# Performance work log

Measured on AMD Instinct MI355X. Metric: run time of the kernel, lower is better.

## Reference

```python
import jax, jax.numpy as jnp
import numpy as np
from jax.ops import segment_sum, segment_max

N = 50000   # nodes
E = 800000  # directed edges
H, C = 4, 64  # GAT heads, per-head channels (hidden_dim//4)
HID = 256
EPS = 1e-5


def setup_inputs() -> dict:
    key = jax.random.key(0)
    ks = jax.random.split(key, 24)
    g = lambda k, shape, fan: jax.random.normal(k, shape, jnp.float32) * (1.0 / np.sqrt(fan))
    inp = {
        'x': jax.random.normal(ks[0], (N, 3), jnp.float32),
        'edge_index': jax.random.randint(ks[1], (2, E), 0, N, jnp.int32),
        # GCNConv 1: 3 -> 64
        'W1': g(ks[2], (3, 64), 3), 'b1': jnp.zeros((64,), jnp.float32),
        # GCNConv 2: 64 -> 128
        'W2': g(ks[3], (64, 128), 64), 'b2': jnp.zeros((128,), jnp.float32),
        # GATConv: 128 -> 4 heads x 64
        'Wg': g(ks[4], (128, H * C), 128),
        'a_src': g(ks[5], (H, C), C), 'a_dst': g(ks[6], (H, C), C),
        'bg': jnp.zeros((H * C,), jnp.float32),
        # LayerNorms
        'ln1_g': jnp.ones((64,), jnp.float32), 'ln1_b': jnp.zeros((64,), jnp.float32),
        'ln2_g': jnp.ones((128,), jnp.float32), 'ln2_b': jnp.zeros((128,), jnp.float32),
        'ln3_g': jnp.ones((HID,), jnp.float32), 'ln3_b': jnp.zeros((HID,), jnp.float32),
        # GlobalAttention gate: Linear(256,256) ReLU Linear(256,1)
        'Wgt1': g(ks[7], (HID, HID), HID), 'bgt1': jnp.zeros((HID,), jnp.float32),
        'Wgt2': g(ks[8], (HID, 1), HID), 'bgt2': jnp.zeros((1,), jnp.float32),
        # output mlp: Linear(256,256) ReLU
        'Wm': g(ks[9], (HID, HID), HID), 'bm': jnp.zeros((HID,), jnp.float32),
    }
    return inp


def _ln(x, g, b):
    mu = x.mean(-1, keepdims=True)
    var = ((x - mu) ** 2).mean(-1, keepdims=True)
    return g * (x - mu) * jax.lax.rsqrt(var + EPS) + b


def reference(x, edge_index, W1, b1, W2, b2, Wg, a_src, a_dst, bg,
              ln1_g, ln1_b, ln2_g, ln2_b, ln3_g, ln3_b,
              Wgt1, bgt1, Wgt2, bgt2, Wm, bm):
    n = x.shape[0]
    loop = jnp.arange(n, dtype=edge_index.dtype)
    src = jnp.concatenate([edge_index[0], loop])  # self-loops added (PyG default)
    dst = jnp.concatenate([edge_index[1], loop])

    # symmetric GCN normalization (deg counts self-loop)
    deg = segment_sum(jnp.ones_like(src, jnp.float32), dst, num_segments=n)
    dinv = jax.lax.rsqrt(jnp.maximum(deg, 1.0))
    norm = (dinv[src] * dinv[dst])[:, None]  # [E+N,1]

    def gcn(h, W, b):
        h = h @ W
        return segment_sum(norm * h[src], dst, num_segments=n) + b

    x1 = _ln(jax.nn.relu(gcn(x, W1, b1)), ln1_g, ln1_b)
    x2 = _ln(jax.nn.relu(gcn(x1, W2, b2)), ln2_g, ln2_b)

    # GATConv: per-head scores, segment-softmax over destination
    h = (x2 @ Wg).reshape(n, H, C)
    s_src = (h * a_src).sum(-1)  # [N,H]
    s_dst = (h * a_dst).sum(-1)
    e = jax.nn.leaky_relu(s_src[src] + s_dst[dst], 0.2)  # [E+N,H]
    m = segment_max(e, dst, num_segments=n)
    ex = jnp.exp(e - m[dst])
    den = segment_sum(ex, dst, num_segments=n)
    alpha = ex / (den[dst] + 1e-16)  # [E+N,H]
    agg = segment_sum(alpha[:, :, None] * h[src], dst, num_segments=n)  # [N,H,C]
    x3 = _ln(agg.reshape(n, H * C) + bg, ln3_g, ln3_b)

    # GlobalAttention pooling (batch=None -> single graph)
    gate = jax.nn.relu(x3 @ Wgt1 + bgt1) @ Wgt2 + bgt2  # [N,1]
    w = jax.nn.softmax(gate, axis=0)
    pooled = (w * x3).sum(0, keepdims=True)  # [1,256]
    out = jax.nn.relu(pooled @ Wm + bm)  # [1,256]
    return out, x3
```

## Files before the change

### kernel.cpp

```cpp
#include <hip/hip_runtime.h>
#include <math.h>

#define NNODES 50000
#define NEDGES 800000

__device__ __forceinline__ float wave_sum(float v) {
#pragma unroll
  for (int o = 32; o > 0; o >>= 1) v += __shfl_xor(v, o, 64);
  return v;
}
__device__ __forceinline__ float wave_max(float v) {
#pragma unroll
  for (int o = 32; o > 0; o >>= 1) v = fmaxf(v, __shfl_xor(v, o, 64));
  return v;
}
template <int NW>
__device__ __forceinline__ float block_sum(float v, float* red) {
  v = wave_sum(v);
  __syncthreads();
  if ((threadIdx.x & 63) == 0) red[threadIdx.x >> 6] = v;
  __syncthreads();
  float s = 0.f;
#pragma unroll
  for (int i = 0; i < NW; i++) s += red[i];
  return s;
}

__device__ __forceinline__ float leaky02(float x) { return x > 0.f ? x : 0.2f * x; }

__device__ __forceinline__ void atomicMaxFloat(float* addr, float val) {
  if (val >= 0.f)
    atomicMax((int*)addr, __float_as_int(val));
  else
    atomicMin((unsigned int*)addr, __float_as_uint(val));
}

__global__ void k_init(int* __restrict__ deg, float* __restrict__ scal,
                       float* __restrict__ pooled) {
  int i = blockIdx.x * blockDim.x + threadIdx.x;
  if (i < NNODES) deg[i] = 0;
  if (i < 256) pooled[i] = 0.f;
  if (i == 0) { scal[0] = -3.0e38f; scal[1] = 0.f; }
}

__global__ void k_deg(const int* __restrict__ dst, int* __restrict__ deg) {
  int e = blockIdx.x * blockDim.x + threadIdx.x;
  if (e < NEDGES) atomicAdd(&deg[dst[e]], 1);
}

__global__ __launch_bounds__(1024) void k_scan(const int* __restrict__ deg,
                                               int* __restrict__ offs,
                                               int* __restrict__ cursor,
                                               float* __restrict__ dinv) {
  __shared__ int lds[1024];
  const int t = threadIdx.x;
  const int chunk = (NNODES + 1023) / 1024;
  int lo = t * chunk, hi = min(lo + chunk, NNODES);
  int s = 0;
  for (int i = lo; i < hi; i++) s += deg[i];
  lds[t] = s;
  __syncthreads();
  for (int off = 1; off < 1024; off <<= 1) {
    int v = (t >= off) ? lds[t - off] : 0;
    __syncthreads();
    lds[t] += v;
    __syncthreads();
  }
  int base = (t > 0) ? lds[t - 1] : 0;
  for (int i = lo; i < hi; i++) {
    int d = deg[i];
    offs[i] = base;
    cursor[i] = base;
    dinv[i] = rsqrtf((float)(d + 1));
    base += d;
  }
  if (t == 1023) offs[NNODES] = lds[1023];
}

__global__ void k_fill(const int* __restrict__ src, const int* __restrict__ dst,
                       int* __restrict__ cursor, int* __restrict__ csr) {
  int e = blockIdx.x * blockDim.x + threadIdx.x;
  if (e >= NEDGES) return;
  int d = dst[e];
  int p = atomicAdd(&cursor[d], 1);
  csr[p] = src[e];
}

__global__ void k_agg3(const float* __restrict__ x, const float* __restrict__ dinv,
                       const int* __restrict__ offs, const int* __restrict__ csr,
                       float* __restrict__ agg0) {
  int n = blockIdx.x * blockDim.x + threadIdx.x;
  if (n >= NNODES) return;
  float di = dinv[n];
  float a0 = di * x[n * 3], a1 = di * x[n * 3 + 1], a2 = di * x[n * 3 + 2];
  int lo = offs[n], hi = offs[n + 1];
  int p = lo;
  int snext = (p < hi) ? csr[p] : 0;
  while (p < hi) {
    int s = snext; p++; if (p < hi) snext = csr[p];
    float w = dinv[s];
    a0 = fmaf(w, x[s * 3], a0);
    a1 = fmaf(w, x[s * 3 + 1], a1);
    a2 = fmaf(w, x[s * 3 + 2], a2);
  }
  agg0[n * 3] = di * a0; agg0[n * 3 + 1] = di * a1; agg0[n * 3 + 2] = di * a2;
}

template <int VEC, int NG>
__global__ __launch_bounds__(64 * NG) void k_agg(const float* __restrict__ h,
                                                 const float* __restrict__ dinv,
                                                 const int* __restrict__ offs,
                                                 const int* __restrict__ csr,
                                                 float* __restrict__ out) {
  __shared__ float lacc[NG][64][VEC + 1];
  const int n = blockIdx.x;
  const int lane = threadIdx.x & 63, g = threadIdx.x >> 6;
  const float di = dinv[n];
  float acc[VEC];
#pragma unroll
  for (int v = 0; v < VEC; v++) acc[v] = 0.f;
  if (g == 0) {
    const float* r = h + (size_t)n * (64 * VEC) + lane * VEC;
#pragma unroll
    for (int v = 0; v < VEC; v++) acc[v] = di * r[v];
  }
  const int lo = offs[n], hi = offs[n + 1];
  int p = lo + g;
  int snext = (p < hi) ? csr[p] : 0;
  while (p < hi) {
    int s = snext; p += NG; if (p < hi) snext = csr[p];
    float w = dinv[s];
    const float* r = h + (size_t)s * (64 * VEC) + lane * VEC;
#pragma unroll
    for (int v = 0; v < VEC; v++) acc[v] = fmaf(w, r[v], acc[v]);
  }
#pragma unroll
  for (int v = 0; v < VEC; v++) lacc[g][lane][v] = acc[v];
  __syncthreads();
  if (g == 0) {
#pragma unroll
    for (int G = 1; G < NG; G++)
#pragma unroll
      for (int v = 0; v < VEC; v++) acc[v] += lacc[G][lane][v];
    float* o = out + (size_t)n * (64 * VEC) + lane * VEC;
#pragma unroll
    for (int v = 0; v < VEC; v++) o[v] = di * acc[v];
  }
}

template <int K, int M, int NT, bool RELU>
__global__ void k_mlp(const float* __restrict__ X, const float* __restrict__ W,
                      const float* __restrict__ b, const float* __restrict__ gam,
                      const float* __restrict__ bet, float* __restrict__ Y) {
  constexpr int NW = M / 64;
  __shared__ float xs[NT * K];
  __shared__ float red[NW];
  const int n0 = blockIdx.x * NT;
  const int j = threadIdx.x;
  const float4* Xt = (const float4*)(X + (size_t)n0 * K);
  for (int i = j; i < NT * K / 4; i += M) ((float4*)xs)[i] = Xt[i];
  __syncthreads();
  float acc[NT];
  float bj = b[j];
#pragma unroll
  for (int r = 0; r < NT; r++) acc[r] = bj;
  for (int k = 0; k < K; k++) {
    float wk = W[k * M + j];
#pragma unroll
    for (int r = 0; r < NT; r++) acc[r] = fmaf(xs[r * K + k], wk, acc[r]);
  }
  float gj = gam[j], btj = bet[j];
  for (int r = 0; r < NT; r++) {
    float a = RELU ? fmaxf(acc[r], 0.f) : acc[r];
    float mu = block_sum<NW>(a, red) * (1.f / M);
    float d = a - mu;
    float var = block_sum<NW>(d * d, red) * (1.f / M);
    Y[(size_t)(n0 + r) * M + j] = fmaf(gj * d, rsqrtf(var + 1e-5f), btj);
  }
}

__global__ void k_uvec(const float* __restrict__ Wg, const float* __restrict__ a_src,
                       const float* __restrict__ a_dst, float* __restrict__ u) {
  const int t = threadIdx.x;
  const int hh = t >> 7, k = t & 127;
  float us = 0.f, ud = 0.f;
  for (int c = 0; c < 64; c++) {
    float w = Wg[k * 256 + hh * 64 + c];
    us = fmaf(w, a_src[hh * 64 + c], us);
    ud = fmaf(w, a_dst[hh * 64 + c], ud);
  }
  u[t] = us;
  u[512 + t] = ud;
}

__global__ __launch_bounds__(256) void k_scores(const float* __restrict__ x2,
                                                const float* __restrict__ u,
                                                float* __restrict__ ssrc,
                                                float* __restrict__ sdst) {
  __shared__ float us[1024];
  const int t = threadIdx.x;
  for (int i = t; i < 1024; i += 256) us[i] = u[i];
  __syncthreads();
  const int n = blockIdx.x * 4 + (t >> 6);
  const int lane = t & 63;
  if (n >= NNODES) return;
  float2 xv = *(const float2*)(x2 + (size_t)n * 128 + lane * 2);
  float d[8];
#pragma unroll
  for (int h = 0; h < 4; h++) {
    d[h] = xv.x * us[h * 128 + lane * 2] + xv.y * us[h * 128 + lane * 2 + 1];
    d[4 + h] = xv.x * us[512 + h * 128 + lane * 2] + xv.y * us[512 + h * 128 + lane * 2 + 1];
  }
#pragma unroll
  for (int o = 32; o > 0; o >>= 1) {
#pragma unroll
    for (int i = 0; i < 8; i++) d[i] += __shfl_xor(d[i], o, 64);
  }
  if (lane == 0) {
    *(float4*)(ssrc + (size_t)n * 4) = make_float4(d[0], d[1], d[2], d[3]);
    *(float4*)(sdst + (size_t)n * 4) = make_float4(d[4], d[5], d[6], d[7]);
  }
}

__global__ __launch_bounds__(256) void k_gatagg(const float* __restrict__ x2,
                                                const float* __restrict__ ssrc,
                                                const float* __restrict__ sdst,
                                                const int* __restrict__ offs,
                                                const int* __restrict__ csr,
                                                float* __restrict__ aggx, int nbase) {
  __shared__ float lm[4][4];
  __shared__ float lden[4][4];
  __shared__ float lacc[4][64][9];
  const int n = nbase + blockIdx.x;
  const int t = threadIdx.x;
  const int lane = t & 63, g = t >> 6;
  const float4 sd = *(const float4*)(sdst + (size_t)n * 4);
  const int lo = offs[n], hi = offs[n + 1];
  float m0 = -3.4e38f, m1 = -3.4e38f, m2 = -3.4e38f, m3 = -3.4e38f;
  float e0x = 0.f, e0y = 0.f, e0z = 0.f, e0w = 0.f;
  if (g == 0) {
    float4 s0 = *(const float4*)(ssrc + (size_t)n * 4);
    e0x = leaky02(s0.x + sd.x); e0y = leaky02(s0.y + sd.y);
    e0z = leaky02(s0.z + sd.z); e0w = leaky02(s0.w + sd.w);
    m0 = e0x; m1 = e0y; m2 = e0z; m3 = e0w;
  }
  for (int p = lo + g; p < hi; p += 4) {
    int s = csr[p];
    float4 ss = *(const float4*)(ssrc + (size_t)s * 4);
    m0 = fmaxf(m0, leaky02(ss.x + sd.x));
    m1 = fmaxf(m1, leaky02(ss.y + sd.y));
    m2 = fmaxf(m2, leaky02(ss.z + sd.z));
    m3 = fmaxf(m3, leaky02(ss.w + sd.w));
  }
  if (lane == 0) { lm[g][0] = m0; lm[g][1] = m1; lm[g][2] = m2; lm[g][3] = m3; }
  __syncthreads();
  const float M0 = fmaxf(fmaxf(lm[0][0], lm[1][0]), fmaxf(lm[2][0], lm[3][0]));
  const float M1 = fmaxf(fmaxf(lm[0][1], lm[1][1]), fmaxf(lm[2][1], lm[3][1]));
  const float M2 = fmaxf(fmaxf(lm[0][2], lm[1][2]), fmaxf(lm[2][2], lm[3][2]));
  const float M3 = fmaxf(fmaxf(lm[0][3], lm[1][3]), fmaxf(lm[2][3], lm[3][3]));
  float den0 = 0.f, den1 = 0.f, den2 = 0.f, den3 = 0.f;
  float a0x = 0.f, a0y = 0.f, a1x = 0.f, a1y = 0.f;
  float a2x = 0.f, a2y = 0.f, a3x = 0.f, a3y = 0.f;
  if (g == 0) {
    float2 xv = *(const float2*)(x2 + (size_t)n * 128 + lane * 2);
    float w;
    w = __expf(e0x - M0); den0 = w; a0x = w * xv.x; a0y = w * xv.y;
    w = __expf(e0y - M1); den1 = w; a1x = w * xv.x; a1y = w * xv.y;
    w = __expf(e0z - M2); den2 = w; a2x = w * xv.x; a2y = w * xv.y;
    w = __expf(e0w - M3); den3 = w; a3x = w * xv.x; a3y = w * xv.y;
  }
  int p = lo + g;
  int snext = (p < hi) ? csr[p] : 0;
  while (p < hi) {
    int s = snext; p += 4; if (p < hi) snext = csr[p];
    float4 ss = *(const float4*)(ssrc + (size_t)s * 4);
    float2 xv = *(const float2*)(x2 + (size_t)s * 128 + lane * 2);
    float w0 = __expf(leaky02(ss.x + sd.x) - M0);
    float w1 = __expf(leaky02(ss.y + sd.y) - M1);
    float w2 = __expf(leaky02(ss.z + sd.z) - M2);
    float w3 = __expf(leaky02(ss.w + sd.w) - M3);
    den0 += w0; den1 += w1; den2 += w2; den3 += w3;
    a0x = fmaf(w0, xv.x, a0x); a0y = fmaf(w0, xv.y, a0y);
    a1x = fmaf(w1, xv.x, a1x); a1y = fmaf(w1, xv.y, a1y);
    a2x = fmaf(w2, xv.x, a2x); a2y = fmaf(w2, xv.y, a2y);
    a3x = fmaf(w3, xv.x, a3x); a3y = fmaf(w3, xv.y, a3y);
  }
  if (lane == 0) { lden[g][0] = den0; lden[g][1] = den1; lden[g][2] = den2; lden[g][3] = den3; }
  lacc[g][lane][0] = a0x; lacc[g][lane][1] = a0y;
  lacc[g][lane][2] = a1x; lacc[g][lane][3] = a1y;
  lacc[g][lane][4] = a2x; lacc[g][lane][5] = a2y;
  lacc[g][lane][6] = a3x; lacc[g][lane][7] = a3y;
  __syncthreads();
  float den = lden[0][g] + lden[1][g] + lden[2][g] + lden[3][g] + 1e-16f;
  float ax = lacc[0][lane][2 * g] + lacc[1][lane][2 * g] + lacc[2][lane][2 * g] + lacc[3][lane][2 * g];
  float ay = lacc[0][lane][2 * g + 1] + lacc[1][lane][2 * g + 1] + lacc[2][lane][2 * g + 1] + lacc[3][lane][2 * g + 1];
  float2 ov; ov.x = ax / den; ov.y = ay / den;
  *(float2*)(aggx + (size_t)blockIdx.x * 512 + g * 128 + lane * 2) = ov;
}

__global__ __launch_bounds__(256) void k_proj(const float* __restrict__ aggx,
                                              const float* __restrict__ Wg,
                                              const float* __restrict__ bg,
                                              const float* __restrict__ gam,
                                              const float* __restrict__ bet,
                                              float* __restrict__ x3, int nbase,
                                              int nrows) {
  __shared__ float xs[16][4 * 132];
  const int r0 = blockIdx.x * 16;
  const int t = threadIdx.x;
  const int cq = t & 63, rq = t >> 6;
  const int h = cq >> 4;
  for (int idx = t; idx < 16 * 128; idx += 256) {
    int r = idx >> 7;
    int p = (idx & 127) << 2;
    int hh = p >> 7, k = p & 127;
    float4 v = (r0 + r < nrows)
                   ? *(const float4*)(aggx + (size_t)(r0 + r) * 512 + p)
                   : make_float4(0.f, 0.f, 0.f, 0.f);
    *(float4*)&xs[r][hh * 132 + k] = v;
  }
  __syncthreads();
  float acc[4][4];
#pragma unroll
  for (int i = 0; i < 4; i++)
#pragma unroll
    for (int j = 0; j < 4; j++) acc[i][j] = 0.f;
  const float4* Wv = (const float4*)Wg;
  for (int k0 = 0; k0 < 128; k0 += 4) {
    float4 xk[4], wk[4];
#pragma unroll
    for (int i = 0; i < 4; i++)
      xk[i] = *(const float4*)&xs[rq * 4 + i][h * 132 + k0];
#pragma unroll
    for (int kk = 0; kk < 4; kk++) wk[kk] = Wv[(size_t)(k0 + kk) * 64 + cq];
#pragma unroll
    for (int kk = 0; kk < 4; kk++) {
      const float* wf = (const float*)&wk[kk];
#pragma unroll
      for (int i = 0; i < 4; i++) {
        const float* xf = (const float*)&xk[i];
        float xv = xf[kk];
#pragma unroll
        for (int j = 0; j < 4; j++) acc[i][j] = fmaf(xv, wf[j], acc[i][j]);
      }
    }
  }
  float4 bgv = *(const float4*)(bg + cq * 4);
  float4 gav = *(const float4*)(gam + cq * 4);
  float4 bev = *(const float4*)(bet + cq * 4);
  const float* bgf = (const float*)&bgv;
  const float* gaf = (const float*)&gav;
  const float* bef = (const float*)&bev;
#pragma unroll
  for (int i = 0; i < 4; i++) {
    float a[4], s = 0.f;
#pragma unroll
    for (int j = 0; j < 4; j++) { a[j] = acc[i][j] + bgf[j]; s += a[j]; }
    float mu = wave_sum(s) * (1.f / 256.f);
    float s2 = 0.f;
#pragma unroll
    for (int j = 0; j < 4; j++) { float d = a[j] - mu; s2 += d * d; }
    float rs = rsqrtf(wave_sum(s2) * (1.f / 256.f) + 1e-5f);
    int r = r0 + rq * 4 + i;
    if (r < nrows) {
      float4 ov;
      ov.x = fmaf(gaf[0] * (a[0] - mu), rs, bef[0]);
      ov.y = fmaf(gaf[1] * (a[1] - mu), rs, bef[1]);
      ov.z = fmaf(gaf[2] * (a[2] - mu), rs, bef[2]);
      ov.w = fmaf(gaf[3] * (a[3] - mu), rs, bef[3]);
      *(float4*)(x3 + (size_t)(nbase + r) * 256 + cq * 4) = ov;
    }
  }
}

__global__ __launch_bounds__(256) void k_gate(const float* __restrict__ x3,
                                              const float* __restrict__ Wgt1,
                                              const float* __restrict__ bgt1,
                                              const float* __restrict__ Wgt2,
                                              const float* __restrict__ bgt2,
                                              float* __restrict__ gate) {
  __shared__ float xs[16][256];
  const int n0 = blockIdx.x * 16;
  const int t = threadIdx.x;
  const int cq = t & 63, rq = t >> 6;
  for (int idx = t; idx < 16 * 64; idx += 256) {
    int r = idx >> 6, p = (idx & 63) << 2;
    *(float4*)&xs[r][p] = *(const float4*)(x3 + (size_t)(n0 + r) * 256 + p);
  }
  __syncthreads();
  float acc[4][4];
#pragma unroll
  for (int i = 0; i < 4; i++)
#pragma unroll
    for (int j = 0; j < 4; j++) acc[i][j] = 0.f;
  const float4* Wv = (const float4*)Wgt1;
  for (int k0 = 0; k0 < 256; k0 += 4) {
    float4 xk[4], wk[4];
#pragma unroll
    for (int i = 0; i < 4; i++) xk[i] = *(const float4*)&xs[rq * 4 + i][k0];
#pragma unroll
    for (int kk = 0; kk < 4; kk++) wk[kk] = Wv[(size_t)(k0 + kk) * 64 + cq];
#pragma unroll
    for (int kk = 0; kk < 4; kk++) {
      const float* wf = (const float*)&wk[kk];
#pragma unroll
      for (int i = 0; i < 4; i++) {
        const float* xf = (const float*)&xk[i];
        float xv = xf[kk];
#pragma unroll
        for (int j = 0; j < 4; j++) acc[i][j] = fmaf(xv, wf[j], acc[i][j]);
      }
    }
  }
  float4 b1v = *(const float4*)(bgt1 + cq * 4);
  float4 w2v = *(const float4*)(Wgt2 + cq * 4);
  const float* b1f = (const float*)&b1v;
  const float* w2f = (const float*)&w2v;
  float b2 = bgt2[0];
#pragma unroll
  for (int i = 0; i < 4; i++) {
    float s = 0.f;
#pragma unroll
    for (int j = 0; j < 4; j++)
      s = fmaf(fmaxf(acc[i][j] + b1f[j], 0.f), w2f[j], s);
    s = wave_sum(s);
    if (cq == 0) gate[n0 + rq * 4 + i] = s + b2;
  }
}

__global__ void k_gmax(const float* __restrict__ gate, float* __restrict__ scal) {
  __shared__ float red[4];
  int i = blockIdx.x * 256 + threadIdx.x;
  float v = (i < NNODES) ? gate[i] : -3.0e38f;
  v = wave_max(v);
  __syncthreads();
  if ((threadIdx.x & 63) == 0) red[threadIdx.x >> 6] = v;
  __syncthreads();
  if (threadIdx.x == 0) {
    float m = fmaxf(fmaxf(red[0], red[1]), fmaxf(red[2], red[3]));
    atomicMaxFloat(&scal[0], m);
  }
}

__global__ void k_pool(const float* __restrict__ x3, const float* __restrict__ gate,
                       const float* __restrict__ scal, float* __restrict__ pooled) {
  const int c = threadIdx.x;
  const float gmax = scal[0];
  float acc = 0.f, zl = 0.f;
  for (int node = blockIdx.x; node < NNODES; node += gridDim.x) {
    float wv = __expf(gate[node] - gmax);
    if (c == 0) zl += wv;
    acc = fmaf(wv, x3[(size_t)node * 256 + c], acc);
  }
  atomicAdd(&pooled[c], acc);
  if (c == 0) atomicAdd((float*)&scal[1], zl);
}

__global__ void k_out(const float* __restrict__ pooled, const float* __restrict__ scal,
                      const float* __restrict__ Wm, const float* __restrict__ bm,
                      float* __restrict__ out) {
  __shared__ float p[256];
  const int j = threadIdx.x;
  p[j] = pooled[j] / scal[1];
  __syncthreads();
  float acc = bm[j];
  for (int k = 0; k < 256; k++) acc = fmaf(p[k], Wm[k * 256 + j], acc);
  out[j] = fmaxf(acc, 0.f);
}

extern "C" void kernel_launch(void* const* d_in, const int* in_sizes, int n_in,
                              void* d_out, int out_size, void* d_ws, size_t ws_size,
                              hipStream_t stream) {
  const float* x     = (const float*)d_in[0];
  const int*   ei    = (const int*)d_in[1];
  const float* W1    = (const float*)d_in[2];
  const float* b1    = (const float*)d_in[3];
  const float* W2    = (const float*)d_in[4];
  const float* b2    = (const float*)d_in[5];
  const float* Wg    = (const float*)d_in[6];
  const float* a_src = (const float*)d_in[7];
  const float* a_dst = (const float*)d_in[8];
  const float* bg    = (const float*)d_in[9];
  const float* ln1g  = (const float*)d_in[10];
  const float* ln1b  = (const float*)d_in[11];
  const float* ln2g  = (const float*)d_in[12];
  const float* ln2b  = (const float*)d_in[13];
  const float* ln3g  = (const float*)d_in[14];
  const float* ln3b  = (const float*)d_in[15];
  const float* Wgt1  = (const float*)d_in[16];
  const float* bgt1  = (const float*)d_in[17];
  const float* Wgt2  = (const float*)d_in[18];
  const float* bgt2  = (const float*)d_in[19];
  const float* Wm    = (const float*)d_in[20];
  const float* bm    = (const float*)d_in[21];

  float* out = (float*)d_out;
  float* x3  = out + 256;

  const int* src = ei;
  const int* dst = ei + NEDGES;

  char* wsb = (char*)d_ws;
  size_t off = 0;
  auto carve = [&](size_t bytes) -> void* {
    void* p = wsb + off;
    off += (bytes + 255) & ~(size_t)255;
    return p;
  };
  int*   deg    = (int*)carve((size_t)NNODES * 4);
  int*   offs   = (int*)carve((size_t)(NNODES + 1) * 4);
  int*   cursor = (int*)carve((size_t)NNODES * 4);
  int*   csr    = (int*)carve((size_t)NEDGES * 4);
  float* dinv   = (float*)carve((size_t)NNODES * 4);
  float* bufA   = (float*)carve((size_t)NNODES * 256 * 4);
  float* x2     = (float*)carve((size_t)NNODES * 128 * 4);
  float* ssrc   = (float*)carve((size_t)NNODES * 4 * 4);
  float* sdst   = (float*)carve((size_t)NNODES * 4 * 4);
  float* u      = (float*)carve(1024 * 4);
  float* gate   = (float*)carve((size_t)NNODES * 4);
  float* pooled = (float*)carve(256 * 4);
  float* scal   = (float*)carve(2 * 4);

  float* x1   = bufA;
  float* agg1 = bufA + (size_t)NNODES * 64;
  float* agg0 = bufA + (size_t)NNODES * 128;
  float* aggx = bufA;

  k_init<<<(NNODES + 255) / 256, 256, 0, stream>>>(deg, scal, pooled);
  k_deg<<<NEDGES / 256, 256, 0, stream>>>(dst, deg);
  k_scan<<<1, 1024, 0, stream>>>(deg, offs, cursor, dinv);
  k_fill<<<NEDGES / 256, 256, 0, stream>>>(src, dst, cursor, csr);

  k_agg3<<<(NNODES + 255) / 256, 256, 0, stream>>>(x, dinv, offs, csr, agg0);
  k_mlp<3, 64, 16, true><<<NNODES / 16, 64, 0, stream>>>(agg0, W1, b1, ln1g, ln1b, x1);

  k_agg<1, 4><<<NNODES, 256, 0, stream>>>(x1, dinv, offs, csr, agg1);
  k_mlp<64, 128, 8, true><<<NNODES / 8, 128, 0, stream>>>(agg1, W2, b2, ln2g, ln2b, x2);

  k_uvec<<<1, 512, 0, stream>>>(Wg, a_src, a_dst, u);
  k_scores<<<(NNODES + 3) / 4, 256, 0, stream>>>(x2, u, ssrc, sdst);
  for (int c = 0; c < 2; c++) {
    int nbase = c * (NNODES / 2);
    int nrows = NNODES / 2;
    k_gatagg<<<nrows, 256, 0, stream>>>(x2, ssrc, sdst, offs, csr, aggx, nbase);
    k_proj<<<(nrows + 15) / 16, 256, 0, stream>>>(aggx, Wg, bg, ln3g, ln3b, x3,
                                                  nbase, nrows);
  }

  k_gate<<<NNODES / 16, 256, 0, stream>>>(x3, Wgt1, bgt1, Wgt2, bgt2, gate);
  k_gmax<<<(NNODES + 255) / 256, 256, 0, stream>>>(gate, scal);
  k_pool<<<256, 256, 0, stream>>>(x3, gate, scal, pooled);
  k_out<<<1, 256, 0, stream>>>(pooled, scal, Wm, bm, out);
}
```

Measured before the change: 922.5 us.

## Replace single-block prefix scan with three-pass multi-block wave-shuffle scan

Replaces the single-block 1024-thread degree scan, in which each thread serially walks about 49 contiguous entries with strided uncoalesced loads, with a three-kernel scan. Per-block sums are computed first, then a one-block scan of the 196 block sums, then a per-block wave-shuffle scan that writes offsets, cursors and dinv. The aim is to spread the scan across many CUs with coalesced accesses, at the cost of two extra kernel launches.

```diff
diff --git a/kernel.cpp b/kernel.cpp
--- a/kernel.cpp
+++ b/kernel.cpp
@@ -3,6 +3,7 @@
 
 #define NNODES 50000
 #define NEDGES 800000
+#define NB 196
 
 __device__ __forceinline__ float wave_sum(float v) {
 #pragma unroll
@@ -12,6 +13,19 @@
 __device__ __forceinline__ float wave_max(float v) {
 #pragma unroll
   for (int o = 32; o > 0; o >>= 1) v = fmaxf(v, __shfl_xor(v, o, 64));
+  return v;
+}
+__device__ __forceinline__ int wave_isum(int v) {
+#pragma unroll
+  for (int o = 32; o > 0; o >>= 1) v += __shfl_xor(v, o, 64);
+  return v;
+}
+__device__ __forceinline__ int wave_iscan(int v, int lane) {
+#pragma unroll
+  for (int o = 1; o < 64; o <<= 1) {
+    int u = __shfl_up(v, o, 64);
+    if (lane >= o) v += u;
+  }
   return v;
 }
 template <int NW>
@@ -48,33 +62,51 @@
   if (e < NEDGES) atomicAdd(&deg[dst[e]], 1);
 }
 
-__global__ __launch_bounds__(1024) void k_scan(const int* __restrict__ deg,
+__global__ __launch_bounds__(256) void k_scan1(const int* __restrict__ deg,
+                                               int* __restrict__ bsum) {
+  __shared__ int red[4];
+  int i = blockIdx.x * 256 + threadIdx.x;
+  int v = (i < NNODES) ? deg[i] : 0;
+  v = wave_isum(v);
+  if ((threadIdx.x & 63) == 0) red[threadIdx.x >> 6] = v;
+  __syncthreads();
+  if (threadIdx.x == 0) bsum[blockIdx.x] = red[0] + red[1] + red[2] + red[3];
+}
+
+__global__ __launch_bounds__(256) void k_scan2(const int* __restrict__ bsum,
+                                               int* __restrict__ bbase) {
+  __shared__ int wsum[4];
+  const int t = threadIdx.x, lane = t & 63, w = t >> 6;
+  int v = (t < NB) ? bsum[t] : 0;
+  int incl = wave_iscan(v, lane);
+  if (lane == 63) wsum[w] = incl;
+  __syncthreads();
+  int wb = 0;
+  for (int k = 0; k < w; k++) wb += wsum[k];
+  if (t < NB) bbase[t] = wb + incl - v;
+}
+
+__global__ __launch_bounds__(256) void k_scan3(const int* __restrict__ deg,
+                                               const int* __restrict__ bbase,
                                                int* __restrict__ offs,
                                                int* __restrict__ cursor,
                                                float* __restrict__ dinv) {
-  __shared__ int lds[1024];
-  const int t = threadIdx.x;
-  const int chunk = (NNODES + 1023) / 1024;
-  int lo = t * chunk, hi = min(lo + chunk, NNODES);
-  int s = 0;
-  for (int i = lo; i < hi; i++) s += deg[i];
-  lds[t] = s;
-  __syncthreads();
-  for (int off = 1; off < 1024; off <<= 1) {
-    int v = (t >= off) ? lds[t - off] : 0;
-    __syncthreads();
-    lds[t] += v;
-    __syncthreads();
-  }
-  int base = (t > 0) ? lds[t - 1] : 0;
-  for (int i = lo; i < hi; i++) {
-    int d = deg[i];
-    offs[i] = base;
-    cursor[i] = base;
+  __shared__ int wsum[4];
+  const int i = blockIdx.x * 256 + threadIdx.x;
+  const int lane = threadIdx.x & 63, w = threadIdx.x >> 6;
+  int d = (i < NNODES) ? deg[i] : 0;
+  int incl = wave_iscan(d, lane);
+  if (lane == 63) wsum[w] = incl;
+  __syncthreads();
+  int wb = 0;
+  for (int k = 0; k < w; k++) wb += wsum[k];
+  int excl = bbase[blockIdx.x] + wb + incl - d;
+  if (i < NNODES) {
+    offs[i] = excl;
+    cursor[i] = excl;
     dinv[i] = rsqrtf((float)(d + 1));
-    base += d;
-  }
-  if (t == 1023) offs[NNODES] = lds[1023];
+    if (i == NNODES - 1) offs[NNODES] = excl + d;
+  }
 }
 
 __global__ void k_fill(const int* __restrict__ src, const int* __restrict__ dst,
@@ -512,6 +544,8 @@
   int*   cursor = (int*)carve((size_t)NNODES * 4);
   int*   csr    = (int*)carve((size_t)NEDGES * 4);
   float* dinv   = (float*)carve((size_t)NNODES * 4);
+  int*   bsum   = (int*)carve(256 * 4);
+  int*   bbase  = (int*)carve(256 * 4);
   float* bufA   = (float*)carve((size_t)NNODES * 256 * 4);
   float* x2     = (float*)carve((size_t)NNODES * 128 * 4);
   float* ssrc   = (float*)carve((size_t)NNODES * 4 * 4);
@@ -528,7 +562,9 @@
 
   k_init<<<(NNODES + 255) / 256, 256, 0, stream>>>(deg, scal, pooled);
   k_deg<<<NEDGES / 256, 256, 0, stream>>>(dst, deg);
-  k_scan<<<1, 1024, 0, stream>>>(deg, offs, cursor, dinv);
+  k_scan1<<<NB, 256, 0, stream>>>(deg, bsum);
+  k_scan2<<<1, 256, 0, stream>>>(bsum, bbase);
+  k_scan3<<<NB, 256, 0, stream>>>(deg, bbase, offs, cursor, dinv);
   k_fill<<<NEDGES / 256, 256, 0, stream>>>(src, dst, cursor, csr);
 
   k_agg3<<<(NNODES + 255) / 256, 256, 0, stream>>>(x, dinv, offs, csr, agg0);
```

Measured after the change: 802.5 us. -13.0%, faster.
